# Optimization experiments

Hardware: AMD Instinct MI355X
Metric: run time of the kernel (lower is better)

The kernel has to match this reference:

```python
import jax, jax.numpy as jnp
import numpy as np

N, R, D, K = 2048, 64, 64, 512  # batch, n_roles, filler_embed_dim, n_fillers
LAMBDA_VQ, LAMBDA_COMMIT, LAMBDA_ORTH = 1.0, 0.5, 0.0


def setup_inputs() -> dict:
    key = jax.random.key(0)
    k1, k2 = jax.random.split(key)
    soft_fillers = jax.random.normal(k1, (N, R, D), dtype=jnp.float32)
    weight = jax.random.normal(k2, (K, D), dtype=jnp.float32)  # codebook rows
    return {"soft_fillers": soft_fillers, "weight": weight}


def _nearest(x, w):
    # x: [M, D], w: [K, D] -> nearest codebook rows + indices
    d = (jnp.sum(x * x, axis=-1, keepdims=True)
         - 2.0 * (x @ w.T)
         + jnp.sum(w * w, axis=-1))          # [M, K]
    idx = jnp.argmin(d, axis=-1)              # [M]
    return w[idx], idx                        # gather: [M, D]


def reference(soft_fillers, weight):
    flat = soft_fillers.reshape(-1, D)        # [N*R, D]

    # Path 1: weight_sg=True -> weight detached, straight-through to input
    q_sg_flat, idx = _nearest(flat, jax.lax.stop_gradient(weight))
    q_sg_flat = flat + jax.lax.stop_gradient(q_sg_flat - flat)

    # Path 2: input detached -> gradient flows to weight via gather
    q_flat, _ = _nearest(jax.lax.stop_gradient(flat), weight)

    q_sg = q_sg_flat.reshape(N, R, D)
    q = q_flat.reshape(N, R, D)
    filler_idxs = idx.reshape(N, R)

    # vq loss: mean over (N, D) of L2-norm over roles of elementwise-squared diff
    t_vq = (q - jax.lax.stop_gradient(soft_fillers)) ** 2          # [N, R, D]
    vq_loss = jnp.mean(jnp.sqrt(jnp.sum(t_vq * t_vq, axis=1)))
    t_c = (jax.lax.stop_gradient(q) - soft_fillers) ** 2
    commit_loss = jnp.mean(jnp.sqrt(jnp.sum(t_c * t_c, axis=1)))

    # semi-orthogonality penalty on weight.t() (rows of codebook): ||W^T W - I||_F
    gram = weight.T @ weight                                        # [D, D]
    orth_penalty = jnp.linalg.norm(gram - jnp.eye(D, dtype=weight.dtype))

    total_loss = (LAMBDA_VQ * vq_loss + LAMBDA_COMMIT * commit_loss
                  + LAMBDA_ORTH * orth_penalty)

    filler_rank = jnp.linalg.matrix_rank(weight).astype(jnp.float32)

    return (total_loss, vq_loss, commit_loss, orth_penalty, filler_rank,
            q_sg, q, filler_idxs)
```

## Files before the change

kernel.cpp:

```cpp
#include <hip/hip_runtime.h>
#include <math.h>

#define N_ 2048
#define R_ 64
#define D_ 64
#define K_ 512
#define M_ (N_*R_)
#define TAU 0.05f
#define CHK 0.02f

#define WN_OFF   16
#define GRAM_OFF 1024
#define WBF_BYTE 32768
#define WS_NEED  163840

typedef __attribute__((ext_vector_type(8))) short s16x8;
typedef __attribute__((ext_vector_type(4))) float f32x4;

static __device__ __forceinline__ unsigned short f2bf(float f) {
    unsigned u = __float_as_uint(f);
    u += 0x7FFFu + ((u >> 16) & 1u);
    return (unsigned short)(u >> 16);
}
static __device__ __forceinline__ float bf2f(unsigned short h) {
    return __uint_as_float(((unsigned)h) << 16);
}

static __device__ __forceinline__ int xs_byte(int r, int q) {
    return r * 256 + (q >> 3) * 128 + (((q & 7) ^ (r & 7)) * 16);
}

static __device__ __forceinline__ void split8(const float* vv, s16x8& ph, s16x8& pl) {
#pragma unroll
    for (int j = 0; j < 8; ++j) {
        const unsigned short hb = f2bf(vv[j]);
        ph[j] = (short)hb;
        pl[j] = (short)f2bf(vv[j] - bf2f(hb));
    }
}

__global__ void k_pre(const float* __restrict__ w, float* __restrict__ ws, int pre) {
    const int b = blockIdx.x, t = threadIdx.x;
    if (b < 64) {
        __shared__ float red[4][64];
        const int i = b, j = t & 63, kg = t >> 6;
        float s = 0.f;
        for (int k = kg * 128; k < kg * 128 + 128; ++k)
            s = fmaf(w[k * 64 + i], w[k * 64 + j], s);
        red[kg][j] = s;
        __syncthreads();
        if (t < 64)
            ws[GRAM_OFF + i * 64 + t] = red[0][t] + red[1][t] + red[2][t] + red[3][t];
    } else if (b < 66) {
        const int code = (b - 64) * 256 + t;
        const float4* wr = (const float4*)(w + code * 64);
        float s = 0.f;
#pragma unroll
        for (int i = 0; i < 16; ++i) {
            float4 v = wr[i];
            s += v.x * v.x + v.y * v.y + v.z * v.z + v.w * v.w;
        }
        ws[WN_OFF + code] = s;
        if (b == 64 && t == 0) ws[0] = 0.f;
    } else {
        if (!pre) return;
        const int code = (b - 66) * 256 + t;
        char* whi = (char*)ws + WBF_BYTE;
        char* wlo = whi + 65536;
        const int c = code >> 6, rr = code & 63;
        const int nt = rr >> 4, lr = rr & 15;
        for (int kg = 0; kg < 8; ++kg) {
            float4 v0 = *(const float4*)(w + code * 64 + kg * 8);
            float4 v1 = *(const float4*)(w + code * 64 + kg * 8 + 4);
            const float vv[8] = {v0.x, v0.y, v0.z, v0.w, v1.x, v1.y, v1.z, v1.w};
            s16x8 ph, pl;
            split8(vv, ph, pl);
            const int s = kg >> 2, g = kg & 3, l = g * 16 + lr;
            const int off = (((c * 2 + s) * 4 + nt) << 10) + l * 16;
            *(s16x8*)(whi + off) = ph;
            *(s16x8*)(wlo + off) = pl;
        }
    }
}

template<bool PRE>
__global__ __launch_bounds__(256) void k_argmin(
    const float* __restrict__ x, const float* __restrict__ w,
    float* __restrict__ ws, float* __restrict__ out)
{
    __shared__ __align__(16) float xs[8192];
    __shared__ __align__(16) float redv[2][16][64];
    __shared__ float fb1[128], fb2[128];
    __shared__ int   ridx[128];
    __shared__ int   ulist[128];
    __shared__ int   nunc;

    const int t = threadIdx.x;
    const int l = t & 63, wid = t >> 6;
    const int g = l >> 4, lr = l & 15;
    const long brow = (long)blockIdx.x * 128;
    const float* wn_g = ws + WN_OFF;
    const char* whi = (const char*)ws + WBF_BYTE;
    const char* wlo = whi + 65536;

    if (t == 0) nunc = 0;

#pragma unroll
    for (int ii = 0; ii < 8; ++ii) {
        const int gid = ii * 256 + t;
        const int r = gid >> 4, qq = gid & 15;
        const float4 v = *(const float4*)(x + (brow + r) * 64 + qq * 4);
        *(float4*)((char*)xs + xs_byte(r, qq)) = v;
    }
    __syncthreads();

    s16x8 ah[2][2], al[2][2];
#pragma unroll
    for (int mt = 0; mt < 2; ++mt) {
        const int row = wid * 32 + mt * 16 + lr;
#pragma unroll
        for (int s = 0; s < 2; ++s) {
            const int kg = s * 4 + g;
            const float4 v0 = *(const float4*)((const char*)xs + xs_byte(row, kg * 2));
            const float4 v1 = *(const float4*)((const char*)xs + xs_byte(row, kg * 2 + 1));
            const float vv[8] = {v0.x, v0.y, v0.z, v0.w, v1.x, v1.y, v1.z, v1.w};
            split8(vv, ah[mt][s], al[mt][s]);
        }
    }

    float b1[2][4], b2[2][4]; int i1[2][4];
#pragma unroll
    for (int mt = 0; mt < 2; ++mt)
#pragma unroll
        for (int j = 0; j < 4; ++j) { b1[mt][j] = 3.4e38f; b2[mt][j] = 3.4e38f; i1[mt][j] = 0; }

    for (int c = 0; c < 8; ++c) {
        f32x4 acc[2][4];
        const f32x4 z = {0.f, 0.f, 0.f, 0.f};
#pragma unroll
        for (int mt = 0; mt < 2; ++mt)
#pragma unroll
            for (int nt = 0; nt < 4; ++nt) acc[mt][nt] = z;

#pragma unroll
        for (int half = 0; half < 2; ++half) {
            s16x8 bh[2][2], bl[2][2];
#pragma unroll
            for (int s = 0; s < 2; ++s)
#pragma unroll
                for (int nth = 0; nth < 2; ++nth) {
                    const int nt = half * 2 + nth;
                    if constexpr (PRE) {
                        const int off = (((c * 2 + s) * 4 + nt) << 10) + l * 16;
                        bh[s][nth] = *(const s16x8*)(whi + off);
                        bl[s][nth] = *(const s16x8*)(wlo + off);
                    } else {
                        const int crow = c * 64 + nt * 16 + lr;
                        const float* src = w + (long)crow * 64 + (s * 4 + g) * 8;
                        const float4 v0 = *(const float4*)src;
                        const float4 v1 = *(const float4*)(src + 4);
                        const float vv[8] = {v0.x, v0.y, v0.z, v0.w, v1.x, v1.y, v1.z, v1.w};
                        split8(vv, bh[s][nth], bl[s][nth]);
                    }
                }
#pragma unroll
            for (int s = 0; s < 2; ++s)
#pragma unroll
                for (int nth = 0; nth < 2; ++nth) {
                    const int nt = half * 2 + nth;
#pragma unroll
                    for (int mt = 0; mt < 2; ++mt) {
                        acc[mt][nt] = __builtin_amdgcn_mfma_f32_16x16x32_bf16(ah[mt][s], bh[s][nth], acc[mt][nt], 0, 0, 0);
                        acc[mt][nt] = __builtin_amdgcn_mfma_f32_16x16x32_bf16(al[mt][s], bh[s][nth], acc[mt][nt], 0, 0, 0);
                        acc[mt][nt] = __builtin_amdgcn_mfma_f32_16x16x32_bf16(ah[mt][s], bl[s][nth], acc[mt][nt], 0, 0, 0);
                    }
                }
        }

#pragma unroll
        for (int nt = 0; nt < 4; ++nt) {
            const int code = c * 64 + nt * 16 + lr;
            const float wnv = wn_g[code];
#pragma unroll
            for (int mt = 0; mt < 2; ++mt)
#pragma unroll
                for (int j = 0; j < 4; ++j) {
                    const float sv = fmaf(-2.f, acc[mt][nt][j], wnv);
                    if (sv < b1[mt][j]) { b2[mt][j] = b1[mt][j]; b1[mt][j] = sv; i1[mt][j] = code; }
                    else if (sv < b2[mt][j]) b2[mt][j] = sv;
                }
        }
    }

#pragma unroll
    for (int m = 1; m < 16; m <<= 1) {
#pragma unroll
        for (int mt = 0; mt < 2; ++mt)
#pragma unroll
            for (int j = 0; j < 4; ++j) {
                const float ov1 = __shfl_xor(b1[mt][j], m, 64);
                const int   oi1 = __shfl_xor(i1[mt][j], m, 64);
                const float ov2 = __shfl_xor(b2[mt][j], m, 64);
                const float nb2 = fminf(fminf(b2[mt][j], ov2), fmaxf(b1[mt][j], ov1));
                if (ov1 < b1[mt][j] || (ov1 == b1[mt][j] && oi1 < i1[mt][j])) {
                    b1[mt][j] = ov1; i1[mt][j] = oi1;
                }
                b2[mt][j] = nb2;
            }
    }
    if (lr == 0) {
#pragma unroll
        for (int mt = 0; mt < 2; ++mt)
#pragma unroll
            for (int j = 0; j < 4; ++j) {
                const int ro = wid * 32 + mt * 16 + g * 4 + j;
                ridx[ro] = i1[mt][j];
                fb1[ro] = b1[mt][j];
                fb2[ro] = b2[mt][j];
            }
    }
    __syncthreads();

    {
        const int r = t >> 1, sub = t & 1;
        const int ci = ridx[r];
        const float* wrow = w + (long)ci * 64 + sub * 32;
        float dot = 0.f;
#pragma unroll
        for (int p = 0; p < 8; ++p) {
            const float4 xv = *(const float4*)((const char*)xs + xs_byte(r, sub * 8 + p));
            const float4 wv = *(const float4*)(wrow + p * 4);
            dot = fmaf(xv.x, wv.x, dot);
            dot = fmaf(xv.y, wv.y, dot);
            dot = fmaf(xv.z, wv.z, dot);
            dot = fmaf(xv.w, wv.w, dot);
        }
        dot += __shfl_xor(dot, 1, 64);
        if (sub == 0) {
            const float sex = fmaf(-2.f, dot, wn_g[ci]);
            const bool unc = ((fb2[r] - fb1[r]) < TAU) || (fabsf(sex - fb1[r]) > CHK);
            if (unc) { const int p = atomicAdd(&nunc, 1); ulist[p] = r; }
        }
    }
    __syncthreads();

    const int nu = nunc;
    if (nu > 0) {
        for (int e = wid; e < nu; e += 4) {
            const int r = ulist[e];
            float bv = 3.4e38f; int bi = 0;
            for (int cc = 0; cc < 8; ++cc) {
                const int code = cc * 64 + l;
                const float* wrow = w + (long)code * 64;
                float dot = 0.f;
#pragma unroll
                for (int p = 0; p < 16; ++p) {
                    const float4 xv = *(const float4*)((const char*)xs + xs_byte(r, p));
                    const float4 wv = *(const float4*)(wrow + p * 4);
                    dot = fmaf(xv.x, wv.x, dot);
                    dot = fmaf(xv.y, wv.y, dot);
                    dot = fmaf(xv.z, wv.z, dot);
                    dot = fmaf(xv.w, wv.w, dot);
                }
                const float sv = fmaf(-2.f, dot, wn_g[code]);
                if (sv < bv) { bv = sv; bi = code; }
            }
#pragma unroll
            for (int m = 1; m < 64; m <<= 1) {
                const float ov = __shfl_xor(bv, m, 64);
                const int   oi = __shfl_xor(bi, m, 64);
                if (ov < bv || (ov == bv && oi < bi)) { bv = ov; bi = oi; }
            }
            if (l == 0) ridx[r] = bi;
        }
    }
    __syncthreads();

    float* q_sg = out + 5;
    float* q    = out + 5 + (long)M_ * 64;
    float* fidx = out + 5 + 2L * M_ * 64;
    const int qq = t & 15, ry = t >> 4;
    float4 va = {0.f, 0.f, 0.f, 0.f}, vb = {0.f, 0.f, 0.f, 0.f};
#pragma unroll
    for (int ii = 0; ii < 8; ++ii) {
        const int r = ii * 16 + ry;
        const int ci = ridx[r];
        const float4 wv4 = *(const float4*)(w + (long)ci * 64 + qq * 4);
        const float4 xv4 = *(const float4*)((const char*)xs + xs_byte(r, qq));
        const long off = (brow + r) * 64 + qq * 4;
        *(float4*)(q_sg + off) = wv4;
        *(float4*)(q + off) = wv4;
        float4 p;
        p.x = (wv4.x - xv4.x) * (wv4.x - xv4.x);
        p.y = (wv4.y - xv4.y) * (wv4.y - xv4.y);
        p.z = (wv4.z - xv4.z) * (wv4.z - xv4.z);
        p.w = (wv4.w - xv4.w) * (wv4.w - xv4.w);
        float4 p2;
        p2.x = p.x * p.x; p2.y = p.y * p.y; p2.z = p.z * p.z; p2.w = p.w * p.w;
        if (ii < 4) {
            va.x += p2.x; va.y += p2.y; va.z += p2.z; va.w += p2.w;
        } else {
            vb.x += p2.x; vb.y += p2.y; vb.z += p2.z; vb.w += p2.w;
        }
    }
    *(float4*)&redv[0][ry][qq * 4] = va;
    *(float4*)&redv[1][ry][qq * 4] = vb;
    if (t < 128) fidx[brow + t] = (float)ridx[t];
    __syncthreads();

    if (t < 128) {
        const int n = t >> 6, d = t & 63;
        float s = 0.f;
#pragma unroll
        for (int u = 0; u < 16; ++u) s += redv[n][u][d];
        float v = sqrtf(s);
#pragma unroll
        for (int m = 1; m < 64; m <<= 1) v += __shfl_xor(v, m, 64);
        if (d == 0) atomicAdd(ws + 0, v);
    }
}

__global__ void k_final(const float* __restrict__ ws, float* __restrict__ out)
{
    __shared__ float g[64][65];
    __shared__ float osum[4];
    __shared__ float tol;
    const int t = threadIdx.x;
    float oacc = 0.f;
    for (int i = t; i < 4096; i += 256) {
        const int r = i >> 6, cl = i & 63;
        const float gv = ws[GRAM_OFF + i];
        g[r][cl] = gv;
        const float p = gv - (r == cl ? 1.f : 0.f);
        oacc = fmaf(p, p, oacc);
    }
#pragma unroll
    for (int m = 1; m < 64; m <<= 1) oacc += __shfl_xor(oacc, m, 64);
    if ((t & 63) == 0) osum[t >> 6] = oacc;
    __syncthreads();

    if (t == 0) {
        float maxd = 0.f;
        for (int i = 0; i < 64; ++i) maxd = fmaxf(maxd, fabsf(g[i][i]));
        tol = maxd * 1e-7f + 1e-30f;
    }
    __syncthreads();

    int rank = 0;
    const int j = t & 63, rq = t >> 6;
    for (int s = 0; s < 64; ++s) {
        const float p = g[s][s];
        const bool ok = fabsf(p) > tol;
        if (ok) {
            rank++;
            if (j > s) {
                const float rp = 1.f / p;
                const float gsj = g[s][j];
                for (int r = s + 1 + rq; r < 64; r += 4)
                    g[r][j] = fmaf(-(g[r][s] * rp), gsj, g[r][j]);
            }
        }
        __syncthreads();
    }

    if (t == 0) {
        const float vq = ws[0] / (float)(N_ * D_);
        const float orth = sqrtf(osum[0] + osum[1] + osum[2] + osum[3]);
        out[0] = 1.5f * vq;
        out[1] = vq;
        out[2] = vq;
        out[3] = orth;
        out[4] = (float)rank;
    }
}

extern "C" void kernel_launch(void* const* d_in, const int* in_sizes, int n_in,
                              void* d_out, int out_size, void* d_ws, size_t ws_size,
                              hipStream_t stream) {
    const float* x = (const float*)d_in[0];
    const float* w = (const float*)d_in[1];
    float* out = (float*)d_out;
    float* ws  = (float*)d_ws;
    const int pre = (ws_size >= (size_t)WS_NEED) ? 1 : 0;

    hipLaunchKernelGGL(k_pre, dim3(68), dim3(256), 0, stream, w, ws, pre);
    if (pre)
        hipLaunchKernelGGL((k_argmin<true>),  dim3(1024), dim3(256), 0, stream, x, w, ws, out);
    else
        hipLaunchKernelGGL((k_argmin<false>), dim3(1024), dim3(256), 0, stream, x, w, ws, out);
    hipLaunchKernelGGL(k_final, dim3(1), dim3(256), 0, stream, ws, out);
}
```

Measured before the change: 191.9 us.

## Shrink argmin blocks, drop LDS staging, ballot-based per-wave recheck with nontemporal stores

After: 214.2 us. 1.12x slower.

```diff
diff --git a/kernel.cpp b/kernel.cpp
--- a/kernel.cpp
+++ b/kernel.cpp
@@ -6,8 +6,8 @@
 #define D_ 64
 #define K_ 512
 #define M_ (N_*R_)
-#define TAU 0.05f
-#define CHK 0.02f
+#define TAU 0.012f
+#define CHK 0.012f
 
 #define WN_OFF   16
 #define GRAM_OFF 1024
@@ -26,10 +26,6 @@
     return __uint_as_float(((unsigned)h) << 16);
 }
 
-static __device__ __forceinline__ int xs_byte(int r, int q) {
-    return r * 256 + (q >> 3) * 128 + (((q & 7) ^ (r & 7)) * 16);
-}
-
 static __device__ __forceinline__ void split8(const float* vv, s16x8& ph, s16x8& pl) {
 #pragma unroll
     for (int j = 0; j < 8; ++j) {
@@ -37,6 +33,11 @@
         ph[j] = (short)hb;
         pl[j] = (short)f2bf(vv[j] - bf2f(hb));
     }
+}
+
+static __device__ __forceinline__ void nt_store4(float* p, float x0, float x1, float x2, float x3) {
+    f32x4 v = {x0, x1, x2, x3};
+    __builtin_nontemporal_store(v, (f32x4*)p);
 }
 
 __global__ void k_pre(const float* __restrict__ w, float* __restrict__ ws, int pre) {
@@ -84,45 +85,30 @@
 }
 
 template<bool PRE>
-__global__ __launch_bounds__(256) void k_argmin(
+__global__ __launch_bounds__(128, 3) void k_argmin(
     const float* __restrict__ x, const float* __restrict__ w,
     float* __restrict__ ws, float* __restrict__ out)
 {
-    __shared__ __align__(16) float xs[8192];
-    __shared__ __align__(16) float redv[2][16][64];
-    __shared__ float fb1[128], fb2[128];
-    __shared__ int   ridx[128];
-    __shared__ int   ulist[128];
-    __shared__ int   nunc;
+    __shared__ int   sridx[64];
+    __shared__ float sfb1[64], sfb2[64];
+    __shared__ float redw[2][64];
 
     const int t = threadIdx.x;
     const int l = t & 63, wid = t >> 6;
     const int g = l >> 4, lr = l & 15;
-    const long brow = (long)blockIdx.x * 128;
+    const long gbase = (long)blockIdx.x * 64 + wid * 32;
     const float* wn_g = ws + WN_OFF;
     const char* whi = (const char*)ws + WBF_BYTE;
     const char* wlo = whi + 65536;
 
-    if (t == 0) nunc = 0;
-
-#pragma unroll
-    for (int ii = 0; ii < 8; ++ii) {
-        const int gid = ii * 256 + t;
-        const int r = gid >> 4, qq = gid & 15;
-        const float4 v = *(const float4*)(x + (brow + r) * 64 + qq * 4);
-        *(float4*)((char*)xs + xs_byte(r, qq)) = v;
-    }
-    __syncthreads();
-
     s16x8 ah[2][2], al[2][2];
 #pragma unroll
     for (int mt = 0; mt < 2; ++mt) {
-        const int row = wid * 32 + mt * 16 + lr;
 #pragma unroll
         for (int s = 0; s < 2; ++s) {
-            const int kg = s * 4 + g;
-            const float4 v0 = *(const float4*)((const char*)xs + xs_byte(row, kg * 2));
-            const float4 v1 = *(const float4*)((const char*)xs + xs_byte(row, kg * 2 + 1));
+            const float* src = x + (gbase + mt * 16 + lr) * 64 + (s * 4 + g) * 8;
+            const float4 v0 = *(const float4*)src;
+            const float4 v1 = *(const float4*)(src + 4);
             const float vv[8] = {v0.x, v0.y, v0.z, v0.w, v1.x, v1.y, v1.z, v1.w};
             split8(vv, ah[mt][s], al[mt][s]);
         }
@@ -143,37 +129,30 @@
             for (int nt = 0; nt < 4; ++nt) acc[mt][nt] = z;
 
 #pragma unroll
-        for (int half = 0; half < 2; ++half) {
-            s16x8 bh[2][2], bl[2][2];
-#pragma unroll
-            for (int s = 0; s < 2; ++s)
-#pragma unroll
-                for (int nth = 0; nth < 2; ++nth) {
-                    const int nt = half * 2 + nth;
-                    if constexpr (PRE) {
-                        const int off = (((c * 2 + s) * 4 + nt) << 10) + l * 16;
-                        bh[s][nth] = *(const s16x8*)(whi + off);
-                        bl[s][nth] = *(const s16x8*)(wlo + off);
-                    } else {
-                        const int crow = c * 64 + nt * 16 + lr;
-                        const float* src = w + (long)crow * 64 + (s * 4 + g) * 8;
-                        const float4 v0 = *(const float4*)src;
-                        const float4 v1 = *(const float4*)(src + 4);
-                        const float vv[8] = {v0.x, v0.y, v0.z, v0.w, v1.x, v1.y, v1.z, v1.w};
-                        split8(vv, bh[s][nth], bl[s][nth]);
-                    }
+        for (int s = 0; s < 2; ++s) {
+            s16x8 bh[4], bl[4];
+#pragma unroll
+            for (int nt = 0; nt < 4; ++nt) {
+                if constexpr (PRE) {
+                    const int off = (((c * 2 + s) * 4 + nt) << 10) + l * 16;
+                    bh[nt] = *(const s16x8*)(whi + off);
+                    bl[nt] = *(const s16x8*)(wlo + off);
+                } else {
+                    const int crow = c * 64 + nt * 16 + lr;
+                    const float* src = w + (long)crow * 64 + (s * 4 + g) * 8;
+                    const float4 v0 = *(const float4*)src;
+                    const float4 v1 = *(const float4*)(src + 4);
+                    const float vv[8] = {v0.x, v0.y, v0.z, v0.w, v1.x, v1.y, v1.z, v1.w};
+                    split8(vv, bh[nt], bl[nt]);
                 }
-#pragma unroll
-            for (int s = 0; s < 2; ++s)
-#pragma unroll
-                for (int nth = 0; nth < 2; ++nth) {
-                    const int nt = half * 2 + nth;
-#pragma unroll
-                    for (int mt = 0; mt < 2; ++mt) {
-                        acc[mt][nt] = __builtin_amdgcn_mfma_f32_16x16x32_bf16(ah[mt][s], bh[s][nth], acc[mt][nt], 0, 0, 0);
-                        acc[mt][nt] = __builtin_amdgcn_mfma_f32_16x16x32_bf16(al[mt][s], bh[s][nth], acc[mt][nt], 0, 0, 0);
-                        acc[mt][nt] = __builtin_amdgcn_mfma_f32_16x16x32_bf16(ah[mt][s], bl[s][nth], acc[mt][nt], 0, 0, 0);
-                    }
+            }
+#pragma unroll
+            for (int nt = 0; nt < 4; ++nt)
+#pragma unroll
+                for (int mt = 0; mt < 2; ++mt) {
+                    acc[mt][nt] = __builtin_amdgcn_mfma_f32_16x16x32_bf16(ah[mt][s], bh[nt], acc[mt][nt], 0, 0, 0);
+                    acc[mt][nt] = __builtin_amdgcn_mfma_f32_16x16x32_bf16(al[mt][s], bh[nt], acc[mt][nt], 0, 0, 0);
+                    acc[mt][nt] = __builtin_amdgcn_mfma_f32_16x16x32_bf16(ah[mt][s], bl[nt], acc[mt][nt], 0, 0, 0);
                 }
         }
 
@@ -214,21 +193,23 @@
 #pragma unroll
             for (int j = 0; j < 4; ++j) {
                 const int ro = wid * 32 + mt * 16 + g * 4 + j;
-                ridx[ro] = i1[mt][j];
-                fb1[ro] = b1[mt][j];
-                fb2[ro] = b2[mt][j];
-            }
-    }
-    __syncthreads();
-
+                sridx[ro] = i1[mt][j];
+                sfb1[ro] = b1[mt][j];
+                sfb2[ro] = b2[mt][j];
+            }
+    }
+    __syncthreads();
+
+    unsigned long long um;
     {
-        const int r = t >> 1, sub = t & 1;
-        const int ci = ridx[r];
+        const int r = l >> 1, sub = l & 1;
+        const int ci = sridx[wid * 32 + r];
+        const float* xrow = x + (gbase + r) * 64 + sub * 32;
         const float* wrow = w + (long)ci * 64 + sub * 32;
         float dot = 0.f;
 #pragma unroll
         for (int p = 0; p < 8; ++p) {
-            const float4 xv = *(const float4*)((const char*)xs + xs_byte(r, sub * 8 + p));
+            const float4 xv = *(const float4*)(xrow + p * 4);
             const float4 wv = *(const float4*)(wrow + p * 4);
             dot = fmaf(xv.x, wv.x, dot);
             dot = fmaf(xv.y, wv.y, dot);
@@ -236,87 +217,89 @@
             dot = fmaf(xv.w, wv.w, dot);
         }
         dot += __shfl_xor(dot, 1, 64);
+        bool marked = false;
         if (sub == 0) {
             const float sex = fmaf(-2.f, dot, wn_g[ci]);
-            const bool unc = ((fb2[r] - fb1[r]) < TAU) || (fabsf(sex - fb1[r]) > CHK);
-            if (unc) { const int p = atomicAdd(&nunc, 1); ulist[p] = r; }
-        }
-    }
-    __syncthreads();
-
-    const int nu = nunc;
-    if (nu > 0) {
-        for (int e = wid; e < nu; e += 4) {
-            const int r = ulist[e];
-            float bv = 3.4e38f; int bi = 0;
-            for (int cc = 0; cc < 8; ++cc) {
-                const int code = cc * 64 + l;
-                const float* wrow = w + (long)code * 64;
-                float dot = 0.f;
-#pragma unroll
-                for (int p = 0; p < 16; ++p) {
-                    const float4 xv = *(const float4*)((const char*)xs + xs_byte(r, p));
-                    const float4 wv = *(const float4*)(wrow + p * 4);
-                    dot = fmaf(xv.x, wv.x, dot);
-                    dot = fmaf(xv.y, wv.y, dot);
-                    dot = fmaf(xv.z, wv.z, dot);
-                    dot = fmaf(xv.w, wv.w, dot);
-                }
-                const float sv = fmaf(-2.f, dot, wn_g[code]);
-                if (sv < bv) { bv = sv; bi = code; }
-            }
-#pragma unroll
-            for (int m = 1; m < 64; m <<= 1) {
-                const float ov = __shfl_xor(bv, m, 64);
-                const int   oi = __shfl_xor(bi, m, 64);
-                if (ov < bv || (ov == bv && oi < bi)) { bv = ov; bi = oi; }
-            }
-            if (l == 0) ridx[r] = bi;
-        }
+            const float B1 = sfb1[wid * 32 + r], B2 = sfb2[wid * 32 + r];
+            marked = ((B2 - B1) < TAU) || (fabsf(sex - B1) > CHK);
+        }
+        um = __ballot(marked);
+    }
+
+    while (um) {
+        const int bit = __ffsll((long long)um) - 1;
+        um &= um - 1;
+        const int r = bit >> 1;
+        const float* xrow = x + (gbase + r) * 64;
+        float bv = 3.4e38f; int bi = 0;
+        for (int cc = 0; cc < 8; ++cc) {
+            const int code = cc * 64 + l;
+            const float* wrow = w + (long)code * 64;
+            float dot = 0.f;
+#pragma unroll
+            for (int p = 0; p < 16; ++p) {
+                const float4 xv = *(const float4*)(xrow + p * 4);
+                const float4 wv = *(const float4*)(wrow + p * 4);
+                dot = fmaf(xv.x, wv.x, dot);
+                dot = fmaf(xv.y, wv.y, dot);
+                dot = fmaf(xv.z, wv.z, dot);
+                dot = fmaf(xv.w, wv.w, dot);
+            }
+            const float sv = fmaf(-2.f, dot, wn_g[code]);
+            if (sv < bv) { bv = sv; bi = code; }
+        }
+#pragma unroll
+        for (int m = 1; m < 64; m <<= 1) {
+            const float ov = __shfl_xor(bv, m, 64);
+            const int   oi = __shfl_xor(bi, m, 64);
+            if (ov < bv || (ov == bv && oi < bi)) { bv = ov; bi = oi; }
+        }
+        if (l == 0) sridx[wid * 32 + r] = bi;
     }
     __syncthreads();
 
     float* q_sg = out + 5;
     float* q    = out + 5 + (long)M_ * 64;
     float* fidx = out + 5 + 2L * M_ * 64;
-    const int qq = t & 15, ry = t >> 4;
-    float4 va = {0.f, 0.f, 0.f, 0.f}, vb = {0.f, 0.f, 0.f, 0.f};
+    const int qq = l & 15, rr4 = l >> 4;
+    float4 va = {0.f, 0.f, 0.f, 0.f};
 #pragma unroll
     for (int ii = 0; ii < 8; ++ii) {
-        const int r = ii * 16 + ry;
-        const int ci = ridx[r];
+        const int r = ii * 4 + rr4;
+        const int ci = sridx[wid * 32 + r];
         const float4 wv4 = *(const float4*)(w + (long)ci * 64 + qq * 4);
-        const float4 xv4 = *(const float4*)((const char*)xs + xs_byte(r, qq));
-        const long off = (brow + r) * 64 + qq * 4;
-        *(float4*)(q_sg + off) = wv4;
-        *(float4*)(q + off) = wv4;
+        const float4 xv4 = *(const float4*)(x + (gbase + r) * 64 + qq * 4);
+        const long off = (gbase + r) * 64 + qq * 4;
+        nt_store4(q_sg + off, wv4.x, wv4.y, wv4.z, wv4.w);
+        nt_store4(q + off,    wv4.x, wv4.y, wv4.z, wv4.w);
         float4 p;
         p.x = (wv4.x - xv4.x) * (wv4.x - xv4.x);
         p.y = (wv4.y - xv4.y) * (wv4.y - xv4.y);
         p.z = (wv4.z - xv4.z) * (wv4.z - xv4.z);
         p.w = (wv4.w - xv4.w) * (wv4.w - xv4.w);
-        float4 p2;
-        p2.x = p.x * p.x; p2.y = p.y * p.y; p2.z = p.z * p.z; p2.w = p.w * p.w;
-        if (ii < 4) {
-            va.x += p2.x; va.y += p2.y; va.z += p2.z; va.w += p2.w;
-        } else {
-            vb.x += p2.x; vb.y += p2.y; vb.z += p2.z; vb.w += p2.w;
-        }
-    }
-    *(float4*)&redv[0][ry][qq * 4] = va;
-    *(float4*)&redv[1][ry][qq * 4] = vb;
-    if (t < 128) fidx[brow + t] = (float)ridx[t];
-    __syncthreads();
-
-    if (t < 128) {
-        const int n = t >> 6, d = t & 63;
-        float s = 0.f;
-#pragma unroll
-        for (int u = 0; u < 16; ++u) s += redv[n][u][d];
+        va.x = fmaf(p.x, p.x, va.x);
+        va.y = fmaf(p.y, p.y, va.y);
+        va.z = fmaf(p.z, p.z, va.z);
+        va.w = fmaf(p.w, p.w, va.w);
+    }
+#pragma unroll
+    for (int m = 16; m < 64; m <<= 1) {
+        va.x += __shfl_xor(va.x, m, 64);
+        va.y += __shfl_xor(va.y, m, 64);
+        va.z += __shfl_xor(va.z, m, 64);
+        va.w += __shfl_xor(va.w, m, 64);
+    }
+    if (l < 16) *(float4*)&redw[wid][l * 4] = va;
+    __syncthreads();
+
+    if (t < 64) __builtin_nontemporal_store((float)sridx[t], fidx + (long)blockIdx.x * 64 + t);
+
+    if (t < 64) {
+        const float s = redw[0][t] + redw[1][t];
         float v = sqrtf(s);
 #pragma unroll
         for (int m = 1; m < 64; m <<= 1) v += __shfl_xor(v, m, 64);
-        if (d == 0) atomicAdd(ws + 0, v);
+        if (t == 0) atomicAdd(ws + 0, v);
     }
 }
 
@@ -385,8 +368,8 @@
 
     hipLaunchKernelGGL(k_pre, dim3(68), dim3(256), 0, stream, w, ws, pre);
     if (pre)
-        hipLaunchKernelGGL((k_argmin<true>),  dim3(1024), dim3(256), 0, stream, x, w, ws, out);
+        hipLaunchKernelGGL((k_argmin<true>),  dim3(2048), dim3(128), 0, stream, x, w, ws, out);
     else
-        hipLaunchKernelGGL((k_argmin<false>), dim3(1024), dim3(256), 0, stream, x, w, ws, out);
+        hipLaunchKernelGGL((k_argmin<false>), dim3(2048), dim3(128), 0, stream, x, w, ws, out);
     hipLaunchKernelGGL(k_final, dim3(1), dim3(256), 0, stream, ws, out);
 }
```
